# Performance work log

Measured on AMD Instinct MI355X. Metric: run time of the kernel, lower is better.

## Reference

```python
import jax, jax.numpy as jnp
import numpy as np

N_USER, N_MOVIE, H, E = 100000, 50000, 512, 500000

def setup_inputs() -> dict:
    key = jax.random.key(0)
    ks = jax.random.split(key, 8)
    z_user = jax.random.normal(ks[0], (N_USER, H), dtype=jnp.float32)
    z_movie = jax.random.normal(ks[1], (N_MOVIE, H), dtype=jnp.float32)
    edge_row = jax.random.randint(ks[2], (E,), 0, N_USER, dtype=jnp.int64)
    edge_col = jax.random.randint(ks[3], (E,), 0, N_MOVIE, dtype=jnp.int64)
    w1 = jax.random.normal(ks[4], (2 * H, H), dtype=jnp.float32) * (1.0 / np.sqrt(2 * H))
    b1 = jax.random.normal(ks[5], (H,), dtype=jnp.float32) * 0.01
    w2 = jax.random.normal(ks[6], (H, 1), dtype=jnp.float32) * (1.0 / np.sqrt(H))
    b2 = jax.random.normal(ks[7], (1,), dtype=jnp.float32) * 0.01
    return {"z_user": z_user, "z_movie": z_movie, "edge_row": edge_row,
            "edge_col": edge_col, "w1": w1, "b1": b1, "w2": w2, "b2": b2}

def reference(z_user, z_movie, edge_row, edge_col, w1, b1, w2, b2):
    # Gather endpoint embeddings and concat -> [E, 2H]
    z = jnp.concatenate([z_user[edge_row], z_movie[edge_col]], axis=-1)
    h = jax.nn.relu(z @ w1 + b1)      # [E, H]
    out = h @ w2 + b2                 # [E, 1]
    return out.reshape(-1)
```

## Files before the change

kernel.cpp:

```cpp
#include <hip/hip_runtime.h>
#include <hip/hip_bf16.h>

typedef __attribute__((ext_vector_type(8))) short bf16x8;
typedef __attribute__((ext_vector_type(4))) float f32x4;

#define HDIM 512
#define GBM 512
#define GBN 128

__device__ __forceinline__ unsigned short f2bf(float f) {
  unsigned u = __float_as_uint(f);
  u += 0x7fffu + ((u >> 16) & 1u);
  return (unsigned short)(u >> 16);
}

__device__ __forceinline__ unsigned int pk_bf(float x, float y) {
  __hip_bfloat162 h = __float22bfloat162_rn(float2{x, y});
  union { __hip_bfloat162 b; unsigned int u; } cv; cv.b = h;
  return cv.u;
}

__device__ __forceinline__ float blo(unsigned int u) { return __uint_as_float(u << 16); }
__device__ __forceinline__ float bhi(unsigned int u) { return __uint_as_float(u & 0xffff0000u); }

__global__ void k_w1t(const float* __restrict__ w1, unsigned short* __restrict__ w1t) {
  int idx = blockIdx.x * 256 + threadIdx.x;
  int k = idx >> 9;
  int n = idx & 511;
  w1t[n * 1024 + k] = f2bf(w1[idx]);
}

__global__ __launch_bounds__(512) void k_gemm(
    const float* __restrict__ zu, int MU,
    const float* __restrict__ zm, int MM,
    const unsigned short* __restrict__ w1t,
    unsigned short* __restrict__ u1, unsigned short* __restrict__ m1,
    int nCH1)
{
  __shared__ unsigned short Bs[2 * GBN * 256];
  const int tid  = threadIdx.x;
  const int lane = tid & 63;
  const int wid  = tid >> 6;
  const int lm = lane & 15, lq = lane >> 4;

  int chunk = blockIdx.x >> 2, panel = blockIdx.x & 3;
  const float* A; unsigned short* C; int M, koff, mbase;
  if (chunk < nCH1) { A = zu; C = u1; M = MU; koff = 0;    mbase = chunk * GBM; }
  else              { A = zm; C = m1; M = MM; koff = HDIM; mbase = (chunk - nCH1) * GBM; }
  const int nbase = panel * GBN;

  auto ldsb = (__attribute__((address_space(3))) char*)&Bs[0];

  #pragma unroll
  for (int i = 0; i < 8; ++i) {
    int f = i * 8192 + tid * 16;
    int col = (f >> 9) & 127, cb = f & 511;
    int kloc = (cb ^ ((col & 7) << 4)) >> 1;
    const unsigned short* src = w1t + (size_t)(nbase + col) * 1024 + koff + kloc;
    __builtin_amdgcn_global_load_lds(
        (const __attribute__((address_space(1))) unsigned int*)src,
        (__attribute__((address_space(3))) unsigned int*)(ldsb + i * 8192 + wid * 1024),
        16, 0, 0);
  }
  __syncthreads();
  #pragma unroll
  for (int i = 8; i < 16; ++i) {
    int f = i * 8192 + tid * 16;
    int col = (f >> 9) & 127, cb = f & 511;
    int kloc = 256 + ((cb ^ ((col & 7) << 4)) >> 1);
    const unsigned short* src = w1t + (size_t)(nbase + col) * 1024 + koff + kloc;
    __builtin_amdgcn_global_load_lds(
        (const __attribute__((address_space(1))) unsigned int*)src,
        (__attribute__((address_space(3))) unsigned int*)(ldsb + i * 8192 + wid * 1024),
        16, 0, 0);
  }

  const float* ap[4];
  #pragma unroll
  for (int mi = 0; mi < 4; ++mi) {
    int row = mbase + wid * 64 + mi * 16 + lm; if (row > M - 1) row = M - 1;
    ap[mi] = A + (size_t)row * HDIM + lq * 8;
  }

  f32x4 acc[4][8];
  #pragma unroll
  for (int i = 0; i < 4; ++i)
    #pragma unroll
    for (int j = 0; j < 8; ++j) acc[i][j] = (f32x4){0.f, 0.f, 0.f, 0.f};

  const char* bsb = (const char*)&Bs[0];
  const int swz = (lm & 7) << 4;

  #pragma unroll 4
  for (int kk = 0; kk < 8; ++kk) {
    bf16x8 bfr[8];
    #pragma unroll
    for (int ni = 0; ni < 8; ++ni)
      bfr[ni] = *(const bf16x8*)(bsb + (ni * 16 + lm) * 512 + ((kk * 64 + lq * 16) ^ swz));
    #pragma unroll
    for (int mi = 0; mi < 4; ++mi) {
      const float4 v0 = *(const float4*)(ap[mi] + kk * 32);
      const float4 v1 = *(const float4*)(ap[mi] + kk * 32 + 4);
      bf16x8 af; unsigned int* aw = (unsigned int*)&af;
      aw[0] = pk_bf(v0.x, v0.y); aw[1] = pk_bf(v0.z, v0.w);
      aw[2] = pk_bf(v1.x, v1.y); aw[3] = pk_bf(v1.z, v1.w);
      #pragma unroll
      for (int ni = 0; ni < 8; ++ni)
        acc[mi][ni] = __builtin_amdgcn_mfma_f32_16x16x32_bf16(af, bfr[ni], acc[mi][ni], 0, 0, 0);
    }
  }
  __syncthreads();
  #pragma unroll 4
  for (int kk = 8; kk < 16; ++kk) {
    bf16x8 bfr[8];
    #pragma unroll
    for (int ni = 0; ni < 8; ++ni)
      bfr[ni] = *(const bf16x8*)(bsb + 65536 + (ni * 16 + lm) * 512 + (((kk & 7) * 64 + lq * 16) ^ swz));
    #pragma unroll
    for (int mi = 0; mi < 4; ++mi) {
      const float4 v0 = *(const float4*)(ap[mi] + kk * 32);
      const float4 v1 = *(const float4*)(ap[mi] + kk * 32 + 4);
      bf16x8 af; unsigned int* aw = (unsigned int*)&af;
      aw[0] = pk_bf(v0.x, v0.y); aw[1] = pk_bf(v0.z, v0.w);
      aw[2] = pk_bf(v1.x, v1.y); aw[3] = pk_bf(v1.z, v1.w);
      #pragma unroll
      for (int ni = 0; ni < 8; ++ni)
        acc[mi][ni] = __builtin_amdgcn_mfma_f32_16x16x32_bf16(af, bfr[ni], acc[mi][ni], 0, 0, 0);
    }
  }

  #pragma unroll
  for (int mi = 0; mi < 4; ++mi)
    #pragma unroll
    for (int ni = 0; ni < 8; ++ni)
      #pragma unroll
      for (int r = 0; r < 4; ++r) {
        int rg = mbase + wid * 64 + mi * 16 + lq * 4 + r;
        int cg = nbase + ni * 16 + lm;
        if (rg < M) C[(size_t)rg * HDIM + cg] = f2bf(acc[mi][ni][r]);
      }
}

__global__ __launch_bounds__(256) void k_edge(const int* __restrict__ er, const int* __restrict__ ec,
    const unsigned short* __restrict__ u1, const unsigned short* __restrict__ m1,
    const float* __restrict__ b1, const float* __restrict__ w2, const float* __restrict__ b2,
    float* __restrict__ out, int E)
{
  const int lane = threadIdx.x & 63;
  const int gwid = blockIdx.x * 4 + (threadIdx.x >> 6);
  const int nw   = gridDim.x * 4;
  const float4 b1a = *(const float4*)&b1[lane * 8];
  const float4 b1b = *(const float4*)&b1[lane * 8 + 4];
  const float4 w2a = *(const float4*)&w2[lane * 8];
  const float4 w2b = *(const float4*)&w2[lane * 8 + 4];
  const float bias2 = b2[0];
  for (int e = gwid * 4; e < E; e += nw * 4) {
    if (e + 3 < E) {
      uint4 ua[4], va[4];
      #pragma unroll
      for (int j = 0; j < 4; ++j) {
        ua[j] = *(const uint4*)&u1[(size_t)er[e + j] * HDIM + lane * 8];
        va[j] = *(const uint4*)&m1[(size_t)ec[e + j] * HDIM + lane * 8];
      }
      float p[4];
      #pragma unroll
      for (int j = 0; j < 4; ++j) {
        float pj = 0.f, s;
        s = blo(ua[j].x) + blo(va[j].x) + b1a.x; s = fmaxf(s, 0.f); pj += s * w2a.x;
        s = bhi(ua[j].x) + bhi(va[j].x) + b1a.y; s = fmaxf(s, 0.f); pj += s * w2a.y;
        s = blo(ua[j].y) + blo(va[j].y) + b1a.z; s = fmaxf(s, 0.f); pj += s * w2a.z;
        s = bhi(ua[j].y) + bhi(va[j].y) + b1a.w; s = fmaxf(s, 0.f); pj += s * w2a.w;
        s = blo(ua[j].z) + blo(va[j].z) + b1b.x; s = fmaxf(s, 0.f); pj += s * w2b.x;
        s = bhi(ua[j].z) + bhi(va[j].z) + b1b.y; s = fmaxf(s, 0.f); pj += s * w2b.y;
        s = blo(ua[j].w) + blo(va[j].w) + b1b.z; s = fmaxf(s, 0.f); pj += s * w2b.z;
        s = bhi(ua[j].w) + bhi(va[j].w) + b1b.w; s = fmaxf(s, 0.f); pj += s * w2b.w;
        p[j] = pj;
      }
      #pragma unroll
      for (int off = 32; off > 0; off >>= 1)
        #pragma unroll
        for (int j = 0; j < 4; ++j) p[j] += __shfl_down(p[j], off, 64);
      if (lane == 0)
        *(float4*)&out[e] = float4{p[0] + bias2, p[1] + bias2, p[2] + bias2, p[3] + bias2};
    } else {
      for (int j = 0; j < 4 && e + j < E; ++j) {
        const uint4 ua = *(const uint4*)&u1[(size_t)er[e + j] * HDIM + lane * 8];
        const uint4 va = *(const uint4*)&m1[(size_t)ec[e + j] * HDIM + lane * 8];
        float pj = 0.f, s;
        s = blo(ua.x) + blo(va.x) + b1a.x; s = fmaxf(s, 0.f); pj += s * w2a.x;
        s = bhi(ua.x) + bhi(va.x) + b1a.y; s = fmaxf(s, 0.f); pj += s * w2a.y;
        s = blo(ua.y) + blo(va.y) + b1a.z; s = fmaxf(s, 0.f); pj += s * w2a.z;
        s = bhi(ua.y) + bhi(va.y) + b1a.w; s = fmaxf(s, 0.f); pj += s * w2a.w;
        s = blo(ua.z) + blo(va.z) + b1b.x; s = fmaxf(s, 0.f); pj += s * w2b.x;
        s = bhi(ua.z) + bhi(va.z) + b1b.y; s = fmaxf(s, 0.f); pj += s * w2b.y;
        s = blo(ua.w) + blo(va.w) + b1b.z; s = fmaxf(s, 0.f); pj += s * w2b.z;
        s = bhi(ua.w) + bhi(va.w) + b1b.w; s = fmaxf(s, 0.f); pj += s * w2b.w;
        #pragma unroll
        for (int off = 32; off > 0; off >>= 1) pj += __shfl_down(pj, off, 64);
        if (lane == 0) out[e + j] = pj + bias2;
      }
    }
  }
}

__global__ __launch_bounds__(256) void k_fallback(const float* __restrict__ zu, const float* __restrict__ zm,
    const int* __restrict__ er, const int* __restrict__ ec, const float* __restrict__ w1,
    const float* __restrict__ b1, const float* __restrict__ w2, const float* __restrict__ b2,
    float* __restrict__ out, int E)
{
  __shared__ float Zs[64][33];
  __shared__ float Ws[32][65];
  __shared__ float outacc[64];
  __shared__ int ridx[64], cidx[64];
  const int tid = threadIdx.x;
  const int ebase = blockIdx.x * 64;
  if (tid < 64) {
    int e = ebase + tid; if (e > E - 1) e = E - 1;
    ridx[tid] = er[e]; cidx[tid] = ec[e];
    outacc[tid] = 0.f;
  }
  const int tx = tid & 15, ty = tid >> 4;
  for (int nt = 0; nt < 8; ++nt) {
    float acc[4][4] = {};
    for (int kc = 0; kc < 32; ++kc) {
      __syncthreads();
      #pragma unroll
      for (int i = 0; i < 8; ++i) {
        int id = i * 256 + tid;
        int rr = id >> 5, cc = id & 31;
        int k = kc * 32 + cc;
        Zs[rr][cc] = (k < 512) ? zu[(size_t)ridx[rr] * 512 + k]
                               : zm[(size_t)cidx[rr] * 512 + (k - 512)];
      }
      #pragma unroll
      for (int i = 0; i < 8; ++i) {
        int id = i * 256 + tid;
        int kk = id >> 6, nn = id & 63;
        Ws[kk][nn] = w1[(size_t)(kc * 32 + kk) * 512 + nt * 64 + nn];
      }
      __syncthreads();
      #pragma unroll
      for (int kk = 0; kk < 32; ++kk) {
        float a0 = Zs[ty*4+0][kk], a1 = Zs[ty*4+1][kk], a2 = Zs[ty*4+2][kk], a3 = Zs[ty*4+3][kk];
        float q0 = Ws[kk][tx*4+0], q1 = Ws[kk][tx*4+1], q2 = Ws[kk][tx*4+2], q3 = Ws[kk][tx*4+3];
        acc[0][0] += a0*q0; acc[0][1] += a0*q1; acc[0][2] += a0*q2; acc[0][3] += a0*q3;
        acc[1][0] += a1*q0; acc[1][1] += a1*q1; acc[1][2] += a1*q2; acc[1][3] += a1*q3;
        acc[2][0] += a2*q0; acc[2][1] += a2*q1; acc[2][2] += a2*q2; acc[2][3] += a2*q3;
        acc[3][0] += a3*q0; acc[3][1] += a3*q1; acc[3][2] += a3*q2; acc[3][3] += a3*q3;
      }
    }
    #pragma unroll
    for (int i = 0; i < 4; ++i) {
      float p = 0.f;
      #pragma unroll
      for (int j = 0; j < 4; ++j) {
        int n = nt * 64 + tx * 4 + j;
        float h = acc[i][j] + b1[n]; h = fmaxf(h, 0.f);
        p += h * w2[n];
      }
      atomicAdd(&outacc[ty * 4 + i], p);
    }
  }
  __syncthreads();
  if (tid < 64 && (ebase + tid) < E) out[ebase + tid] = outacc[tid] + b2[0];
}

extern "C" void kernel_launch(void* const* d_in, const int* in_sizes, int n_in,
                              void* d_out, int out_size, void* d_ws, size_t ws_size,
                              hipStream_t stream)
{
  const float* z_user  = (const float*)d_in[0];
  const float* z_movie = (const float*)d_in[1];
  const int*   erow    = (const int*)d_in[2];
  const int*   ecol    = (const int*)d_in[3];
  const float* w1      = (const float*)d_in[4];
  const float* b1      = (const float*)d_in[5];
  const float* w2      = (const float*)d_in[6];
  const float* b2      = (const float*)d_in[7];
  float* out = (float*)d_out;

  const int NU = in_sizes[0] / HDIM;
  const int NM = in_sizes[1] / HDIM;
  const int E  = in_sizes[2];

  const size_t need = ((size_t)NU * HDIM + (size_t)NM * HDIM + (size_t)1024 * 512) * 2;
  if (ws_size >= need) {
    unsigned short* u1  = (unsigned short*)d_ws;
    unsigned short* m1  = u1 + (size_t)NU * HDIM;
    unsigned short* w1t = m1 + (size_t)NM * HDIM;
    const int nCH1 = (NU + GBM - 1) / GBM;
    const int nCH2 = (NM + GBM - 1) / GBM;
    k_w1t<<<(1024 * 512) / 256, 256, 0, stream>>>(w1, w1t);
    k_gemm<<<(nCH1 + nCH2) * 4, 512, 0, stream>>>(z_user, NU, z_movie, NM, w1t, u1, m1, nCH1);
    k_edge<<<2048, 256, 0, stream>>>(erow, ecol, u1, m1, b1, w2, b2, out, E);
  } else {
    k_fallback<<<(E + 63) / 64, 256, 0, stream>>>(z_user, z_movie, erow, ecol, w1, b1, w2, b2, out, E);
  }
}
```

Baseline: 676.9 us.

## Drop LDS staging of W1 in node GEMM; use 128x256 tiles with 2x4 wave grid

Rewrites the per-node projection GEMM. It no longer copies a 128-column W1 panel into shared memory and no longer has the block-wide barrier. Each wave now reads its B fragments directly from global memory (through L2), with blocks tiled as 128 rows by 256 columns over a 2D grid and waves arranged 2x4. A operands for all four row tiles are loaded before conversion to give more loads in flight. Dropping the 128KB LDS footprint and the barriers should raise occupancy and simplify the schedule. In exchange, every wave re-reads W1 from cache, and each fp32 A row is now re-read by only two column blocks instead of four.

```diff
diff --git a/kernel.cpp b/kernel.cpp
--- a/kernel.cpp
+++ b/kernel.cpp
@@ -5,8 +5,8 @@
 typedef __attribute__((ext_vector_type(4))) float f32x4;
 
 #define HDIM 512
-#define GBM 512
-#define GBN 128
+#define BM 128
+#define BN 256
 
 __device__ __forceinline__ unsigned short f2bf(float f) {
   unsigned u = __float_as_uint(f);
@@ -35,108 +35,68 @@
     const float* __restrict__ zm, int MM,
     const unsigned short* __restrict__ w1t,
     unsigned short* __restrict__ u1, unsigned short* __restrict__ m1,
-    int nCH1)
-{
-  __shared__ unsigned short Bs[2 * GBN * 256];
-  const int tid  = threadIdx.x;
-  const int lane = tid & 63;
-  const int wid  = tid >> 6;
+    int nMB1)
+{
+  const int lane = threadIdx.x & 63;
+  const int wid  = threadIdx.x >> 6;
+  const int wm = wid & 1, wn = wid >> 1;
   const int lm = lane & 15, lq = lane >> 4;
 
-  int chunk = blockIdx.x >> 2, panel = blockIdx.x & 3;
-  const float* A; unsigned short* C; int M, koff, mbase;
-  if (chunk < nCH1) { A = zu; C = u1; M = MU; koff = 0;    mbase = chunk * GBM; }
-  else              { A = zm; C = m1; M = MM; koff = HDIM; mbase = (chunk - nCH1) * GBM; }
-  const int nbase = panel * GBN;
-
-  auto ldsb = (__attribute__((address_space(3))) char*)&Bs[0];
-
-  #pragma unroll
-  for (int i = 0; i < 8; ++i) {
-    int f = i * 8192 + tid * 16;
-    int col = (f >> 9) & 127, cb = f & 511;
-    int kloc = (cb ^ ((col & 7) << 4)) >> 1;
-    const unsigned short* src = w1t + (size_t)(nbase + col) * 1024 + koff + kloc;
-    __builtin_amdgcn_global_load_lds(
-        (const __attribute__((address_space(1))) unsigned int*)src,
-        (__attribute__((address_space(3))) unsigned int*)(ldsb + i * 8192 + wid * 1024),
-        16, 0, 0);
-  }
-  __syncthreads();
-  #pragma unroll
-  for (int i = 8; i < 16; ++i) {
-    int f = i * 8192 + tid * 16;
-    int col = (f >> 9) & 127, cb = f & 511;
-    int kloc = 256 + ((cb ^ ((col & 7) << 4)) >> 1);
-    const unsigned short* src = w1t + (size_t)(nbase + col) * 1024 + koff + kloc;
-    __builtin_amdgcn_global_load_lds(
-        (const __attribute__((address_space(1))) unsigned int*)src,
-        (__attribute__((address_space(3))) unsigned int*)(ldsb + i * 8192 + wid * 1024),
-        16, 0, 0);
-  }
-
-  const float* ap[4];
+  const float* A; unsigned short* C; int M, koff, mb = blockIdx.y;
+  if (mb < nMB1) { A = zu; C = u1; M = MU; koff = 0; }
+  else           { A = zm; C = m1; M = MM; koff = HDIM; mb -= nMB1; }
+  const int nbase = blockIdx.x * BN;
+  const int mbase = mb * BM;
+
+  const float* ab[4];
   #pragma unroll
   for (int mi = 0; mi < 4; ++mi) {
-    int row = mbase + wid * 64 + mi * 16 + lm; if (row > M - 1) row = M - 1;
-    ap[mi] = A + (size_t)row * HDIM + lq * 8;
-  }
-
-  f32x4 acc[4][8];
+    int row = mbase + wm * 64 + mi * 16 + lm; if (row > M - 1) row = M - 1;
+    ab[mi] = A + (size_t)row * HDIM + lq * 8;
+  }
+  const unsigned short* bb[4];
+  #pragma unroll
+  for (int ni = 0; ni < 4; ++ni) {
+    int col = nbase + wn * 64 + ni * 16 + lm;
+    bb[ni] = w1t + (size_t)col * 1024 + koff + lq * 8;
+  }
+
+  f32x4 acc[4][4];
   #pragma unroll
   for (int i = 0; i < 4; ++i)
     #pragma unroll
-    for (int j = 0; j < 8; ++j) acc[i][j] = (f32x4){0.f, 0.f, 0.f, 0.f};
-
-  const char* bsb = (const char*)&Bs[0];
-  const int swz = (lm & 7) << 4;
-
-  #pragma unroll 4
-  for (int kk = 0; kk < 8; ++kk) {
-    bf16x8 bfr[8];
-    #pragma unroll
-    for (int ni = 0; ni < 8; ++ni)
-      bfr[ni] = *(const bf16x8*)(bsb + (ni * 16 + lm) * 512 + ((kk * 64 + lq * 16) ^ swz));
+    for (int j = 0; j < 4; ++j) acc[i][j] = (f32x4){0.f, 0.f, 0.f, 0.f};
+
+  #pragma unroll 2
+  for (int s = 0; s < 16; ++s) {
+    bf16x8 bfr[4];
+    #pragma unroll
+    for (int ni = 0; ni < 4; ++ni) bfr[ni] = *(const bf16x8*)(bb[ni] + s * 32);
+    float4 v0[4], v1[4];
     #pragma unroll
     for (int mi = 0; mi < 4; ++mi) {
-      const float4 v0 = *(const float4*)(ap[mi] + kk * 32);
-      const float4 v1 = *(const float4*)(ap[mi] + kk * 32 + 4);
+      v0[mi] = *(const float4*)(ab[mi] + s * 32);
+      v1[mi] = *(const float4*)(ab[mi] + s * 32 + 4);
+    }
+    #pragma unroll
+    for (int mi = 0; mi < 4; ++mi) {
       bf16x8 af; unsigned int* aw = (unsigned int*)&af;
-      aw[0] = pk_bf(v0.x, v0.y); aw[1] = pk_bf(v0.z, v0.w);
-      aw[2] = pk_bf(v1.x, v1.y); aw[3] = pk_bf(v1.z, v1.w);
-      #pragma unroll
-      for (int ni = 0; ni < 8; ++ni)
+      aw[0] = pk_bf(v0[mi].x, v0[mi].y); aw[1] = pk_bf(v0[mi].z, v0[mi].w);
+      aw[2] = pk_bf(v1[mi].x, v1[mi].y); aw[3] = pk_bf(v1[mi].z, v1[mi].w);
+      #pragma unroll
+      for (int ni = 0; ni < 4; ++ni)
         acc[mi][ni] = __builtin_amdgcn_mfma_f32_16x16x32_bf16(af, bfr[ni], acc[mi][ni], 0, 0, 0);
     }
   }
-  __syncthreads();
-  #pragma unroll 4
-  for (int kk = 8; kk < 16; ++kk) {
-    bf16x8 bfr[8];
-    #pragma unroll
-    for (int ni = 0; ni < 8; ++ni)
-      bfr[ni] = *(const bf16x8*)(bsb + 65536 + (ni * 16 + lm) * 512 + (((kk & 7) * 64 + lq * 16) ^ swz));
-    #pragma unroll
-    for (int mi = 0; mi < 4; ++mi) {
-      const float4 v0 = *(const float4*)(ap[mi] + kk * 32);
-      const float4 v1 = *(const float4*)(ap[mi] + kk * 32 + 4);
-      bf16x8 af; unsigned int* aw = (unsigned int*)&af;
-      aw[0] = pk_bf(v0.x, v0.y); aw[1] = pk_bf(v0.z, v0.w);
-      aw[2] = pk_bf(v1.x, v1.y); aw[3] = pk_bf(v1.z, v1.w);
-      #pragma unroll
-      for (int ni = 0; ni < 8; ++ni)
-        acc[mi][ni] = __builtin_amdgcn_mfma_f32_16x16x32_bf16(af, bfr[ni], acc[mi][ni], 0, 0, 0);
-    }
-  }
 
   #pragma unroll
   for (int mi = 0; mi < 4; ++mi)
     #pragma unroll
-    for (int ni = 0; ni < 8; ++ni)
+    for (int ni = 0; ni < 4; ++ni)
       #pragma unroll
       for (int r = 0; r < 4; ++r) {
-        int rg = mbase + wid * 64 + mi * 16 + lq * 4 + r;
-        int cg = nbase + ni * 16 + lm;
+        int rg = mbase + wm * 64 + mi * 16 + lq * 4 + r;
+        int cg = nbase + wn * 64 + ni * 16 + lm;
         if (rg < M) C[(size_t)rg * HDIM + cg] = f2bf(acc[mi][ni][r]);
       }
 }
@@ -288,10 +248,10 @@
     unsigned short* u1  = (unsigned short*)d_ws;
     unsigned short* m1  = u1 + (size_t)NU * HDIM;
     unsigned short* w1t = m1 + (size_t)NM * HDIM;
-    const int nCH1 = (NU + GBM - 1) / GBM;
-    const int nCH2 = (NM + GBM - 1) / GBM;
+    const int nMB1 = (NU + BM - 1) / BM;
+    const int nMB2 = (NM + BM - 1) / BM;
     k_w1t<<<(1024 * 512) / 256, 256, 0, stream>>>(w1, w1t);
-    k_gemm<<<(nCH1 + nCH2) * 4, 512, 0, stream>>>(z_user, NU, z_movie, NM, w1t, u1, m1, nCH1);
+    k_gemm<<<dim3(HDIM / BN, nMB1 + nMB2), 512, 0, stream>>>(z_user, NU, z_movie, NM, w1t, u1, m1, nMB1);
     k_edge<<<2048, 256, 0, stream>>>(erow, ecol, u1, m1, b1, w2, b2, out, E);
   } else {
     k_fallback<<<(E + 63) / 64, 256, 0, stream>>>(z_user, z_movie, erow, ecol, w1, b1, w2, b2, out, E);
```

New measurement: 855.8 us. 26.4% more time.
